# Optimization experiments

Measured on AMD Instinct MI355X. Metric: run time of the kernel, lower is better.

Reference implementation:

```python
import math
import jax, jax.numpy as jnp
import numpy as np

N_NODES = 4096
N_EDGES = 16384
N_EFEAT = 16384
L = 8          # mem_token
DIM = 512
HEAD = 8
NL = 2         # mid_num_layers
ROPE_THETA = 10000.0


def _rms(x, w, eps=1e-6):
    v = jnp.mean(jnp.square(x), axis=-1, keepdims=True)
    return x * jax.lax.rsqrt(v + eps) * w


def _rope_cos_sin(seq_len, d, theta):
    inv = 1.0 / (theta ** (jnp.arange(0, d, 2, dtype=jnp.float32) / d))
    f = jnp.outer(jnp.arange(seq_len, dtype=jnp.float32), inv)  # [L, d/2]
    emb = jnp.concatenate([f, f], axis=-1)                       # [L, d]
    return jnp.cos(emb), jnp.sin(emb)


def _rot_half(x):
    h = x.shape[-1] // 2
    return jnp.concatenate([-x[..., h:], x[..., :h]], axis=-1)


def setup_inputs() -> dict:
    key = jax.random.key(0)
    ks = jax.random.split(key, 12)
    s = 0.02
    return {
        "hidden_states": jax.random.normal(ks[0], (N_NODES + N_EFEAT, L * DIM), jnp.float32),
        "edge_index": jax.random.randint(ks[1], (2, N_EDGES), 0, N_NODES),
        "edge_map": jax.random.randint(ks[2], (N_EDGES,), 0, N_EFEAT),
        "num_node_feat": N_NODES,
        "W_qkv": jax.random.normal(ks[3], (NL, DIM, 3 * DIM), jnp.float32) * s,
        "W_e": jax.random.normal(ks[4], (NL, DIM, 2 * DIM), jnp.float32) * s,
        "W_o": jax.random.normal(ks[5], (NL, DIM, DIM), jnp.float32) * s,
        "x_norm_w": jnp.ones((NL, DIM), jnp.float32),
        "xe_norm_w": jnp.ones((NL, DIM), jnp.float32),
        "post_norm_w": jnp.ones((NL, DIM), jnp.float32),
        "ff_W1": jax.random.normal(ks[6], (NL, DIM, 2 * DIM), jnp.float32) * s,
        "ff_b1": jnp.zeros((NL, 2 * DIM), jnp.float32),
        "ff_W2": jax.random.normal(ks[7], (NL, 2 * DIM, DIM), jnp.float32) * s,
        "ff_b2": jnp.zeros((NL, DIM), jnp.float32),
    }


def reference(hidden_states, edge_index, edge_map, num_node_feat,
              W_qkv, W_e, W_o, x_norm_w, xe_norm_w, post_norm_w,
              ff_W1, ff_b1, ff_W2, ff_b2):
    n_layers, dim = W_qkv.shape[0], W_qkv.shape[1]
    n_tot = hidden_states.shape[0]
    seq = hidden_states.shape[1] // dim           # mem_token
    d = dim // HEAD                               # d_model per head
    N = int(num_node_feat)
    src, dst = edge_index[0], edge_index[1]
    cos, sin = _rope_cos_sin(seq, d, ROPE_THETA)
    cos = cos[None, :, None, :]   # [1, L, 1, d]
    sin = sin[None, :, None, :]
    inv_sqrt_d = 1.0 / math.sqrt(d)

    h = hidden_states.reshape(n_tot, seq, dim)
    for l in range(n_layers):
        x = h[:N]                        # [N, L, dim]
        xe = h[N:][edge_map]             # [E, L, dim]
        res = x
        xn = _rms(x, x_norm_w[l])
        xen = _rms(xe, xe_norm_w[l])
        q, k, v = jnp.split(jnp.einsum('nld,de->nle', xn, W_qkv[l]), 3, axis=-1)
        ek, ev = jnp.split(jnp.einsum('eld,df->elf', xen, W_e[l]), 2, axis=-1)
        # gather per-edge, fuse edge features into key/value
        qi = q[dst].reshape(-1, seq, HEAD, d)
        kj = (k[src] + ek).reshape(-1, seq, HEAD, d)
        vj = (v[src] + ev).reshape(-1, seq, HEAD, d)
        # rotary over memory-token positions
        qi = qi * cos + _rot_half(qi) * sin
        kj = kj * cos + _rot_half(kj) * sin
        alpha = jnp.einsum('elhd,elhd->elh', qi, kj) * inv_sqrt_d  # [E, L, H]
        # segment softmax over incoming edges of each destination node
        m = jax.ops.segment_max(alpha, dst, num_segments=N)
        m = jnp.where(jnp.isfinite(m), m, 0.0)
        a = jnp.exp(alpha - m[dst])
        s = jax.ops.segment_sum(a, dst, num_segments=N)
        a = a / (s[dst] + 1e-16)
        out_e = (vj * a[..., None]).reshape(-1, seq, dim)          # [E, L, dim]
        agg = jax.ops.segment_sum(out_e, dst, num_segments=N)      # [N, L, dim]
        out = res + jnp.einsum('nld,de->nle', agg, W_o[l])
        res2 = out
        o = _rms(out, post_norm_w[l])
        ff = jnp.einsum('nlf,fd->nld',
                        jax.nn.relu(jnp.einsum('nld,df->nlf', o, ff_W1[l]) + ff_b1[l]),
                        ff_W2[l]) + ff_b2[l]
        out = res2 + ff
        h = jnp.concatenate([out, h[N:]], axis=0)
    return h
```

## Files before the change

kernel.cpp:

```cpp
#include <hip/hip_runtime.h>

typedef unsigned short u16;
typedef unsigned int   u32;
typedef u16   u16x8 __attribute__((ext_vector_type(8)));
typedef __bf16 bf16x8 __attribute__((ext_vector_type(8)));
typedef float f32x4 __attribute__((ext_vector_type(4)));
typedef float f32x4v __attribute__((ext_vector_type(4)));

#define N_NODES 4096
#define N_EDGES 16384
#define N_EFEAT 16384
#define SEQ 8
#define DIM 512
#define NLAYER 2
#define NROWS_X (N_NODES*SEQ)
#define NROWS_E (N_EDGES*SEQ)

__device__ __forceinline__ float b2f(u16 u){ return __uint_as_float(((u32)u)<<16); }
__device__ __forceinline__ u16 f2b(float f){ u32 b=__float_as_uint(f); b += 0x7FFFu + ((b>>16)&1u); return (u16)(b>>16); }

__device__ __forceinline__ void gl16(const u16* g, u16* l) {
    __builtin_amdgcn_global_load_lds((const __attribute__((address_space(1))) void*)g,
                                     (__attribute__((address_space(3))) void*)l, 16, 0, 0);
}

__global__ void k_tf(const float* __restrict__ src, u16* __restrict__ dst,
                     const float* __restrict__ fold, int K, int N)
{
    int idx = blockIdx.x * 256 + threadIdx.x;
    if (idx >= K * N) return;
    int c = idx / N, j = idx - c * N;
    float v = src[idx];
    if (fold) v *= fold[c];
    dst[(size_t)j * K + c] = f2b(v);
}

__global__ void k_rowprep(const float* __restrict__ src, u16* __restrict__ dst,
                          float* __restrict__ ssout)
{
    int row  = blockIdx.x * 4 + (threadIdx.x >> 6);
    int lane = threadIdx.x & 63;
    const float* p = src + (size_t)row * DIM;
    f32x4v v0 = *(const f32x4v*)(p + lane * 8);
    f32x4v v1 = *(const f32x4v*)(p + lane * 8 + 4);
    float ss = v0[0]*v0[0]+v0[1]*v0[1]+v0[2]*v0[2]+v0[3]*v0[3]
             + v1[0]*v1[0]+v1[1]*v1[1]+v1[2]*v1[2]+v1[3]*v1[3];
    #pragma unroll
    for (int d = 1; d < 64; d <<= 1) ss += __shfl_xor(ss, d);
    if (lane == 0) ssout[row] = ss;
    u16x8 o;
    #pragma unroll
    for (int i = 0; i < 4; ++i) o[i] = f2b(v0[i]);
    #pragma unroll
    for (int i = 0; i < 4; ++i) o[4+i] = f2b(v1[i]);
    *(u16x8*)(dst + (size_t)row * DIM + lane * 8) = o;
}

__global__ void k_mark(const int* __restrict__ emap, int* __restrict__ flag)
{
    int e = blockIdx.x * 256 + threadIdx.x;
    if (e < N_EDGES) flag[emap[e]] = 1;
}
__global__ void k_scanf(const int* __restrict__ flag, int* __restrict__ newid,
                        int* __restrict__ ulist, int* __restrict__ ucnt)
{
    __shared__ int part[256];
    int t = threadIdx.x;
    int base = t * 64;
    int loc[64]; int s = 0;
    #pragma unroll
    for (int i = 0; i < 64; ++i) { loc[i] = s; s += flag[base + i]; }
    part[t] = s; __syncthreads();
    for (int d = 1; d < 256; d <<= 1) {
        int v = (t >= d) ? part[t - d] : 0;
        __syncthreads();
        part[t] += v;
        __syncthreads();
    }
    int pre = (t == 0) ? 0 : part[t - 1];
    #pragma unroll
    for (int i = 0; i < 64; ++i) {
        int m = base + i;
        int id = pre + loc[i];
        newid[m] = id;
        if (flag[m]) ulist[id] = m;
    }
    if (t == 255) ucnt[0] = part[255];
}
__global__ void k_fidx(const int* __restrict__ emap, const int* __restrict__ newid,
                       int* __restrict__ fidx)
{
    int e = blockIdx.x * 256 + threadIdx.x;
    if (e < N_EDGES) fidx[e] = newid[emap[e]];
}
__global__ void k_featprep(const float* __restrict__ hidden, const int* __restrict__ ulist,
                           const int* __restrict__ ucnt,
                           u16* __restrict__ fbf, float* __restrict__ ssout)
{
    int fr = blockIdx.x * 4 + (threadIdx.x >> 6);
    if (fr >= ucnt[0] * SEQ) return;
    int lane = threadIdx.x & 63;
    int j = fr >> 3, l = fr & 7;
    const float* p = hidden + ((size_t)(N_NODES + ulist[j]) * SEQ + l) * DIM;
    f32x4v v0 = *(const f32x4v*)(p + lane * 8);
    f32x4v v1 = *(const f32x4v*)(p + lane * 8 + 4);
    float ss = v0[0]*v0[0]+v0[1]*v0[1]+v0[2]*v0[2]+v0[3]*v0[3]
             + v1[0]*v1[0]+v1[1]*v1[1]+v1[2]*v1[2]+v1[3]*v1[3];
    #pragma unroll
    for (int d = 1; d < 64; d <<= 1) ss += __shfl_xor(ss, d);
    if (lane == 0) ssout[fr] = ss;
    u16x8 o;
    #pragma unroll
    for (int i = 0; i < 4; ++i) o[i] = f2b(v0[i]);
    #pragma unroll
    for (int i = 0; i < 4; ++i) o[4+i] = f2b(v1[i]);
    *(u16x8*)(fbf + (size_t)fr * DIM + lane * 8) = o;
}

__global__ void k_count(const int* __restrict__ dstA, int* __restrict__ cnt)
{
    int e = blockIdx.x * 256 + threadIdx.x;
    if (e < N_EDGES) atomicAdd(&cnt[dstA[e]], 1);
}
__global__ void k_scan(const int* __restrict__ cnt, int* __restrict__ off)
{
    __shared__ int part[256];
    int t = threadIdx.x;
    int base = t * 16;
    int loc[16]; int s = 0;
    #pragma unroll
    for (int i = 0; i < 16; ++i) { loc[i] = s; s += cnt[base + i]; }
    part[t] = s; __syncthreads();
    for (int d = 1; d < 256; d <<= 1) {
        int v = (t >= d) ? part[t - d] : 0;
        __syncthreads();
        part[t] += v;
        __syncthreads();
    }
    int pre = (t == 0) ? 0 : part[t - 1];
    #pragma unroll
    for (int i = 0; i < 16; ++i) off[base + i] = pre + loc[i];
    if (t == 255) off[N_NODES] = part[255];
}
__global__ void k_fill(const int* __restrict__ dstA, const int* __restrict__ off,
                       int* __restrict__ cur, int* __restrict__ elist)
{
    int e = blockIdx.x * 256 + threadIdx.x;
    if (e < N_EDGES) {
        int d = dstA[e];
        int pos = off[d] + atomicAdd(&cur[d], 1);
        elist[pos] = e;
    }
}

#define GEMM_BODY(BID, A_, B_, N_, K_, GX_, MROWS_, SSIN_, BIAS_, RELU_, RESH_, SSOUT_, OUTF_, OUTH_) \
{                                                                                   \
    int tid  = threadIdx.x;                                                         \
    int lane = tid & 63, wid = tid >> 6;                                            \
    int xcd  = (BID) & 7;                                                           \
    int ii_  = (BID) >> 3;                                                          \
    int colt = ii_ % (GX_);                                                         \
    int rowt = (ii_ / (GX_)) * 8 + xcd;                                             \
    int row0 = rowt * 128, col0 = colt * 128;                                       \
    if ((MROWS_) && row0 >= (MROWS_)[0] * SEQ) return;                              \
    int r0 = wid * 32 + (lane >> 2);                                                \
    int r1 = r0 + 16;                                                               \
    int ce0 = ((lane & 3) * 8) ^ (((r0 >> 1) & 3) << 3);                            \
    int ce1 = ((lane & 3) * 8) ^ (((r1 >> 1) & 3) << 3);                            \
    const u16* ga0 = (A_) + (size_t)(row0 + r0) * (K_) + ce0;                       \
    const u16* ga1 = (A_) + (size_t)(row0 + r1) * (K_) + ce1;                       \
    const u16* gb0 = (B_) + (size_t)(col0 + r0) * (K_) + ce0;                       \
    const u16* gb1 = (B_) + (size_t)(col0 + r1) * (K_) + ce1;                       \
    f32x4 acc[4][4];                                                                \
    _Pragma("unroll")                                                               \
    for (int m = 0; m < 4; ++m)                                                     \
        _Pragma("unroll")                                                           \
        for (int n = 0; n < 4; ++n) { f32x4 z = {0.f,0.f,0.f,0.f}; acc[m][n] = z; } \
    int wr = wid >> 1, wc = wid & 1;                                                \
    int m15 = lane & 15, g = lane >> 4;                                             \
    int arow_l = wr * 64 + m15;                                                     \
    int brow_l = wc * 64 + m15;                                                     \
    int ksw = (g * 8) ^ (((m15 >> 1) & 3) << 3);                                    \
    int NT = (K_) / 32;                                                             \
    {                                                                               \
        gl16(ga0, &ldsA[0][wid * 1024]);                                            \
        gl16(ga1, &ldsA[0][wid * 1024 + 512]);                                      \
        gl16(gb0, &ldsB[0][wid * 1024]);                                            \
        gl16(gb1, &ldsB[0][wid * 1024 + 512]);                                      \
    }                                                                               \
    int cur = 0;                                                                    \
    for (int kt = 0; kt < NT; ++kt) {                                               \
        __syncthreads();                                                            \
        if (kt + 1 < NT) {                                                          \
            int ko = (kt + 1) * 32, bf_ = cur ^ 1;                                  \
            gl16(ga0 + ko, &ldsA[bf_][wid * 1024]);                                 \
            gl16(ga1 + ko, &ldsA[bf_][wid * 1024 + 512]);                           \
            gl16(gb0 + ko, &ldsB[bf_][wid * 1024]);                                 \
            gl16(gb1 + ko, &ldsB[bf_][wid * 1024 + 512]);                           \
        }                                                                           \
        bf16x8 af[4], bfr[4];                                                       \
        _Pragma("unroll")                                                           \
        for (int m = 0; m < 4; ++m)                                                 \
            af[m] = *(const bf16x8*)&ldsA[cur][(arow_l + m * 16) * 32 + ksw];       \
        _Pragma("unroll")                                                           \
        for (int n = 0; n < 4; ++n)                                                 \
            bfr[n] = *(const bf16x8*)&ldsB[cur][(brow_l + n * 16) * 32 + ksw];      \
        _Pragma("unroll")                                                           \
        for (int m = 0; m < 4; ++m)                                                 \
            _Pragma("unroll")                                                       \
            for (int n = 0; n < 4; ++n)                                             \
                acc[m][n] = __builtin_amdgcn_mfma_f32_16x16x32_bf16(af[m], bfr[n], acc[m][n], 0, 0, 0); \
        cur ^= 1;                                                                   \
    }                                                                               \
    _Pragma("unroll")                                                               \
    for (int m = 0; m < 4; ++m) {                                                   \
        _Pragma("unroll")                                                           \
        for (int j = 0; j < 4; ++j) {                                               \
            int row = row0 + wr * 64 + m * 16 + g * 4 + j;                          \
            float sc = 0.f;                                                         \
            if (SSIN_) sc = rsqrtf((SSIN_)[row] * (1.f / (float)DIM) + 1e-6f);      \
            float ssa = 0.f;                                                        \
            _Pragma("unroll")                                                       \
            for (int n = 0; n < 4; ++n) {                                           \
                int col = col0 + wc * 64 + n * 16 + m15;                            \
                float v = acc[m][n][j];                                             \
                if (SSIN_) v *= sc;                                                 \
                if (BIAS_) v += (BIAS_)[col];                                       \
                if (RELU_) v = fmaxf(v, 0.f);                                       \
                if (RESH_) v += b2f((RESH_)[(size_t)row * (N_) + col]);             \
                if (OUTF_) (OUTF_)[(size_t)row * (N_) + col] = v;                   \
                if (OUTH_) (OUTH_)[(size_t)row * (N_) + col] = f2b(v);              \
                ssa += v * v;                                                       \
            }                                                                       \
            if (SSOUT_) {                                                           \
                ssa += __shfl_xor(ssa, 1);                                          \
                ssa += __shfl_xor(ssa, 2);                                          \
                ssa += __shfl_xor(ssa, 4);                                          \
                ssa += __shfl_xor(ssa, 8);                                          \
                if (m15 == 0) atomicAdd(&(SSOUT_)[row], ssa);                       \
            }                                                                       \
        }                                                                           \
    }                                                                               \
}

__global__ __launch_bounds__(256, 2) void k_gemm(
    const u16* __restrict__ A, const u16* __restrict__ B,
    int M, int N, int K, int gx, const int* __restrict__ mrows,
    const float* __restrict__ ssin, const float* __restrict__ bias, int relu,
    const u16* __restrict__ resH, float* __restrict__ ssout,
    float* __restrict__ outF, u16* __restrict__ outH)
{
    __shared__ u16 ldsA[2][128 * 32];
    __shared__ u16 ldsB[2][128 * 32];
    GEMM_BODY(blockIdx.x, A, B, N, K, gx, mrows, ssin, bias, relu, resH, ssout, outF, outH)
}

__global__ __launch_bounds__(256, 2) void k_gemm2(
    int nb0,
    const u16* __restrict__ A0, const u16* __restrict__ B0,
    int N0, int K0, int gx0, const int* __restrict__ mrows0,
    const float* __restrict__ ssin0, const float* __restrict__ bias0, int relu0,
    const u16* __restrict__ resH0, float* __restrict__ ssout0,
    float* __restrict__ outF0, u16* __restrict__ outH0,
    const u16* __restrict__ A1, const u16* __restrict__ B1,
    int N1, int K1, int gx1, const int* __restrict__ mrows1,
    const float* __restrict__ ssin1, const float* __restrict__ bias1, int relu1,
    const u16* __restrict__ resH1, float* __restrict__ ssout1,
    float* __restrict__ outF1, u16* __restrict__ outH1)
{
    __shared__ u16 ldsA[2][128 * 32];
    __shared__ u16 ldsB[2][128 * 32];
    if ((int)blockIdx.x < nb0) {
        GEMM_BODY(blockIdx.x, A0, B0, N0, K0, gx0, mrows0, ssin0, bias0, relu0, resH0, ssout0, outF0, outH0)
    } else {
        int bid = blockIdx.x - nb0;
        GEMM_BODY(bid, A1, B1, N1, K1, gx1, mrows1, ssin1, bias1, relu1, resH1, ssout1, outF1, outH1)
    }
}

__global__ __launch_bounds__(256, 2) void k_attn(
    const u16* __restrict__ qkv, const u16* __restrict__ ekv,
    const int* __restrict__ srcA, const int* __restrict__ fidx,
    const int* __restrict__ off, const int* __restrict__ elist,
    u16* __restrict__ agg)
{
    int n = blockIdx.x;
    int t = threadIdx.x;
    int pair = t >> 2, sub = t & 3;
    int l = pair >> 3, hd = pair & 7;
    int doff = hd * 64 + sub * 16;

    size_t qrow = ((size_t)n * SEQ + l) * 1536;
    float qi[16];
    {
        u16x8 qa = *(const u16x8*)&qkv[qrow + doff];
        u16x8 qb = *(const u16x8*)&qkv[qrow + doff + 8];
        #pragma unroll
        for (int i = 0; i < 8; ++i) { qi[i] = b2f(qa[i]); qi[i + 8] = b2f(qb[i]); }
    }

    float mrun = -INFINITY, s = 0.f;
    float av[16];
    #pragma unroll
    for (int i = 0; i < 16; ++i) av[i] = 0.f;

    int e0 = off[n], e1 = off[n + 1];
    for (int ii = e0; ii < e1; ++ii) {
        int e = elist[ii];
        int es = srcA[e];
        size_t krow = ((size_t)es * SEQ + l) * 1536 + 512;
        size_t erow = ((size_t)fidx[e] * SEQ + l) * 1024;

        u16x8 ka = *(const u16x8*)&qkv[krow + doff];
        u16x8 kb = *(const u16x8*)&qkv[krow + doff + 8];
        u16x8 ea = *(const u16x8*)&ekv[erow + doff];
        u16x8 eb = *(const u16x8*)&ekv[erow + doff + 8];

        float dot = 0.f;
        #pragma unroll
        for (int i = 0; i < 8; ++i) {
            dot += qi[i]     * (b2f(ka[i]) + b2f(ea[i]));
            dot += qi[i + 8] * (b2f(kb[i]) + b2f(eb[i]));
        }
        dot += __shfl_xor(dot, 1);
        dot += __shfl_xor(dot, 2);
        float alpha = dot * 0.125f;

        float mn = fmaxf(mrun, alpha);
        float f = expf(mrun - mn);
        float p = expf(alpha - mn);
        s = s * f + p;

        u16x8 va  = *(const u16x8*)&qkv[krow + 512 + doff];
        u16x8 vb  = *(const u16x8*)&qkv[krow + 512 + doff + 8];
        u16x8 eva = *(const u16x8*)&ekv[erow + 512 + doff];
        u16x8 evb = *(const u16x8*)&ekv[erow + 512 + doff + 8];
        #pragma unroll
        for (int i = 0; i < 8; ++i) {
            av[i]     = av[i]     * f + p * (b2f(va[i]) + b2f(eva[i]));
            av[i + 8] = av[i + 8] * f + p * (b2f(vb[i]) + b2f(evb[i]));
        }
        mrun = mn;
    }

    float inv = 1.f / (s + 1e-16f);
    size_t orow = ((size_t)n * SEQ + l) * DIM + doff;
    #pragma unroll
    for (int i = 0; i < 16; ++i) agg[orow + i] = f2b(av[i] * inv);
}

extern "C" void kernel_launch(void* const* d_in, const int* in_sizes, int n_in,
                              void* d_out, int out_size, void* d_ws, size_t ws_size,
                              hipStream_t stream)
{
    const float* hidden = (const float*)d_in[0];
    const int*   eidx   = (const int*)d_in[1];
    const int*   srcA   = eidx;
    const int*   dstA   = eidx + N_EDGES;
    const int*   emap   = (const int*)d_in[2];
    const float* W_qkv  = (const float*)d_in[4];
    const float* W_e    = (const float*)d_in[5];
    const float* W_o    = (const float*)d_in[6];
    const float* xw     = (const float*)d_in[7];
    const float* xew    = (const float*)d_in[8];
    const float* pw     = (const float*)d_in[9];
    const float* W1     = (const float*)d_in[10];
    const float* b1     = (const float*)d_in[11];
    const float* W2     = (const float*)d_in[12];
    const float* b2     = (const float*)d_in[13];

    char* w = (char*)d_ws;
    auto alloc = [&](size_t bytes) { char* p = w; w += (bytes + 255) & ~(size_t)255; return p; };
    u16*  WtQKV  = (u16*)alloc((size_t)NLAYER * 1536 * 512 * 2);
    u16*  WtE    = (u16*)alloc((size_t)NLAYER * 1024 * 512 * 2);
    u16*  WtO    = (u16*)alloc((size_t)NLAYER * 512 * 512 * 2);
    u16*  Wt1    = (u16*)alloc((size_t)NLAYER * 1024 * 512 * 2);
    u16*  Wt2    = (u16*)alloc((size_t)NLAYER * 512 * 1024 * 2);
    float* ssx0  = (float*)alloc((size_t)NROWS_X * 4);
    float* ssx1  = (float*)alloc((size_t)NROWS_X * 4);
    float* ssp0  = (float*)alloc((size_t)NROWS_X * 4);
    float* ssp1  = (float*)alloc((size_t)NROWS_X * 4);
    float* s_f   = (float*)alloc((size_t)NROWS_E * 4);
    int*  cnt    = (int*)alloc((N_NODES + 1) * 4);
    int*  off    = (int*)alloc((N_NODES + 1) * 4);
    int*  cur    = (int*)alloc(N_NODES * 4);
    int*  elist  = (int*)alloc(N_EDGES * 4);
    int*  flag   = (int*)alloc(N_EFEAT * 4);
    int*  newid  = (int*)alloc(N_EFEAT * 4);
    int*  ulist  = (int*)alloc(N_EFEAT * 4);
    int*  fidx   = (int*)alloc(N_EDGES * 4);
    int*  ucnt   = (int*)alloc(256);
    u16*  hb     = (u16*)alloc((size_t)NROWS_X * DIM * 2);
    u16*  ob     = (u16*)alloc((size_t)NROWS_X * DIM * 2);
    u16*  fbf    = (u16*)alloc((size_t)NROWS_E * DIM * 2);
    u16*  qkv    = (u16*)alloc((size_t)NROWS_X * 1536 * 2);
    u16*  aggB   = (u16*)alloc((size_t)NROWS_X * DIM * 2);
    u16*  ffmid  = (u16*)alloc((size_t)NROWS_X * 1024 * 2);
    u16*  ekv    = (u16*)((float*)d_out + (size_t)NROWS_X * DIM);
    float* ssx[2] = { ssx0, ssx1 };
    float* ssp[2] = { ssp0, ssp1 };

    for (int l = 0; l < NLAYER; ++l) {
        k_tf<<<(512*1536 + 255)/256, 256, 0, stream>>>(W_qkv + (size_t)l*512*1536, WtQKV + (size_t)l*1536*512, xw  + l*512, 512, 1536);
        k_tf<<<(512*1024 + 255)/256, 256, 0, stream>>>(W_e   + (size_t)l*512*1024, WtE   + (size_t)l*1024*512, xew + l*512, 512, 1024);
        k_tf<<<(512*512  + 255)/256, 256, 0, stream>>>(W_o   + (size_t)l*512*512,  WtO   + (size_t)l*512*512,  nullptr,    512, 512);
        k_tf<<<(512*1024 + 255)/256, 256, 0, stream>>>(W1    + (size_t)l*512*1024, Wt1   + (size_t)l*1024*512, pw  + l*512, 512, 1024);
        k_tf<<<(1024*512 + 255)/256, 256, 0, stream>>>(W2    + (size_t)l*1024*512, Wt2   + (size_t)l*512*1024, nullptr,    1024, 512);
    }
    hipMemsetAsync(ssx1, 0, NROWS_X * 4, stream);
    hipMemsetAsync(ssp0, 0, NROWS_X * 4, stream);
    hipMemsetAsync(ssp1, 0, NROWS_X * 4, stream);
    hipMemsetAsync(flag, 0, N_EFEAT * 4, stream);
    k_mark<<<N_EDGES/256, 256, 0, stream>>>(emap, flag);
    k_scanf<<<1, 256, 0, stream>>>(flag, newid, ulist, ucnt);
    k_fidx<<<N_EDGES/256, 256, 0, stream>>>(emap, newid, fidx);
    k_featprep<<<NROWS_E/4, 256, 0, stream>>>(hidden, ulist, ucnt, fbf, s_f);
    hipMemsetAsync(cnt, 0, (N_NODES + 1) * 4, stream);
    hipMemsetAsync(cur, 0, N_NODES * 4, stream);
    k_count<<<N_EDGES/256, 256, 0, stream>>>(dstA, cnt);
    k_scan<<<1, 256, 0, stream>>>(cnt, off);
    k_fill<<<N_EDGES/256, 256, 0, stream>>>(dstA, off, cur, elist);
    k_rowprep<<<NROWS_X/4, 256, 0, stream>>>(hidden, hb, ssx0);

    const int nbQ = (NROWS_X/128)*(1536/128);
    const int nbE = (NROWS_E/128)*(1024/128);

    for (int l = 0; l < NLAYER; ++l) {
        int last = (l == NLAYER - 1);
        k_gemm2<<<nbQ + nbE, 256, 0, stream>>>(nbQ,
            hb, WtQKV + (size_t)l*1536*512, 1536, 512, 1536/128, nullptr,
            ssx[l], nullptr, 0, nullptr, nullptr, nullptr, qkv,
            fbf, WtE + (size_t)l*1024*512, 1024, 512, 1024/128, ucnt,
            s_f, nullptr, 0, nullptr, nullptr, nullptr, ekv);
        k_attn<<<N_NODES, 256, 0, stream>>>(qkv, ekv, srcA, fidx, off, elist, aggB);
        k_gemm<<<(NROWS_X/128)*(512/128), 256, 0, stream>>>(aggB, WtO + (size_t)l*512*512,
            NROWS_X, 512, 512, 512/128, nullptr,
            nullptr, nullptr, 0, hb, ssp[l], nullptr, ob);
        k_gemm<<<(NROWS_X/128)*(1024/128), 256, 0, stream>>>(ob, Wt1 + (size_t)l*1024*512,
            NROWS_X, 1024, 512, 1024/128, nullptr,
            ssp[l], b1 + l*1024, 1, nullptr, nullptr, nullptr, ffmid);
        k_gemm<<<(NROWS_X/128)*(512/128), 256, 0, stream>>>(ffmid, Wt2 + (size_t)l*512*1024,
            NROWS_X, 512, 1024, 512/128, nullptr,
            nullptr, b2 + l*512, 0, ob,
            last ? nullptr : ssx[1],
            last ? (float*)d_out : nullptr,
            last ? nullptr : hb);
    }

    hipMemcpyAsync((float*)d_out + (size_t)NROWS_X * DIM, hidden + (size_t)NROWS_X * DIM,
                   (size_t)N_EDGES * SEQ * DIM * 4, hipMemcpyDeviceToDevice, stream);
}
```

Before: 1.330 ms.

## Fuse setup launches and overlap the edge-feature tail copy with the W_o GEMM

Ten per-layer weight transpose launches and four memsets become a single multi-segment kernel. The node-row and edge-feature prep kernels become one launch. The large device-to-device copy of the untouched edge-feature rows was a trailing memcpy; it now runs as extra blocks of the last layer's W_o GEMM, so the copy overlaps with compute. The copy reuses the output region that held the ekv scratch, which is safe only because attention has already consumed ekv by that point. The trade-off is that copy blocks compete with the GEMM for memory bandwidth.

```diff
diff --git a/kernel.cpp b/kernel.cpp
--- a/kernel.cpp
+++ b/kernel.cpp
@@ -24,36 +24,78 @@
                                      (__attribute__((address_space(3))) void*)l, 16, 0, 0);
 }
 
-__global__ void k_tf(const float* __restrict__ src, u16* __restrict__ dst,
-                     const float* __restrict__ fold, int K, int N)
-{
-    int idx = blockIdx.x * 256 + threadIdx.x;
-    if (idx >= K * N) return;
-    int c = idx / N, j = idx - c * N;
-    float v = src[idx];
-    if (fold) v *= fold[c];
-    dst[(size_t)j * K + c] = f2b(v);
-}
-
-__global__ void k_rowprep(const float* __restrict__ src, u16* __restrict__ dst,
-                          float* __restrict__ ssout)
-{
-    int row  = blockIdx.x * 4 + (threadIdx.x >> 6);
+#define TF_SEG(CNT, SRC, DST, FOLD, KK, NN)                                   \
+    if (b < (CNT)) {                                                          \
+        int idx = b * 256 + threadIdx.x;                                      \
+        int c = idx / (NN), j = idx - c * (NN);                               \
+        float v = (SRC)[idx];                                                 \
+        if (FOLD) v *= (FOLD)[c];                                             \
+        (DST)[(size_t)j * (KK) + c] = f2b(v);                                 \
+        return;                                                               \
+    }                                                                         \
+    b -= (CNT);
+
+__global__ void k_tfall(const float* __restrict__ Wqkv, const float* __restrict__ We,
+                        const float* __restrict__ Wo,   const float* __restrict__ W1,
+                        const float* __restrict__ W2,
+                        const float* __restrict__ xw, const float* __restrict__ xew,
+                        const float* __restrict__ pw,
+                        u16* __restrict__ WtQKV, u16* __restrict__ WtE, u16* __restrict__ WtO,
+                        u16* __restrict__ Wt1, u16* __restrict__ Wt2,
+                        float* __restrict__ z0, float* __restrict__ z1,
+                        float* __restrict__ z2, int* __restrict__ zf)
+{
+    int b = blockIdx.x;
+    if (b >= 20480) {
+        b -= 20480;
+        if (b < 128) { z0[b * 256 + threadIdx.x] = 0.f; return; }
+        b -= 128;
+        if (b < 128) { z1[b * 256 + threadIdx.x] = 0.f; return; }
+        b -= 128;
+        if (b < 128) { z2[b * 256 + threadIdx.x] = 0.f; return; }
+        b -= 128;
+        zf[b * 256 + threadIdx.x] = 0; return;
+    }
+    int l = b / 10240; b -= l * 10240;
+    TF_SEG(3072, Wqkv + (size_t)l*512*1536, WtQKV + (size_t)l*1536*512, xw  + l*512, 512, 1536)
+    TF_SEG(2048, We   + (size_t)l*512*1024, WtE   + (size_t)l*1024*512, xew + l*512, 512, 1024)
+    TF_SEG(1024, Wo   + (size_t)l*512*512,  WtO   + (size_t)l*512*512,  (const float*)nullptr, 512, 512)
+    TF_SEG(2048, W1   + (size_t)l*512*1024, Wt1   + (size_t)l*1024*512, pw  + l*512, 512, 1024)
+    TF_SEG(2048, W2   + (size_t)l*1024*512, Wt2   + (size_t)l*512*1024, (const float*)nullptr, 1024, 512)
+}
+
+__global__ void k_prep(const float* __restrict__ hidden, const int* __restrict__ ulist,
+                       const int* __restrict__ ucnt,
+                       u16* __restrict__ fbf, float* __restrict__ s_f,
+                       u16* __restrict__ hb, float* __restrict__ ssx0)
+{
     int lane = threadIdx.x & 63;
-    const float* p = src + (size_t)row * DIM;
+    const float* p;
+    u16* dst; float* ssout; int orow;
+    if (blockIdx.x < NROWS_E / 4) {
+        int fr = blockIdx.x * 4 + (threadIdx.x >> 6);
+        if (fr >= ucnt[0] * SEQ) return;
+        int j = fr >> 3, l = fr & 7;
+        p = hidden + ((size_t)(N_NODES + ulist[j]) * SEQ + l) * DIM;
+        dst = fbf + (size_t)fr * DIM; ssout = s_f; orow = fr;
+    } else {
+        int row = (blockIdx.x - NROWS_E / 4) * 4 + (threadIdx.x >> 6);
+        p = hidden + (size_t)row * DIM;
+        dst = hb + (size_t)row * DIM; ssout = ssx0; orow = row;
+    }
     f32x4v v0 = *(const f32x4v*)(p + lane * 8);
     f32x4v v1 = *(const f32x4v*)(p + lane * 8 + 4);
     float ss = v0[0]*v0[0]+v0[1]*v0[1]+v0[2]*v0[2]+v0[3]*v0[3]
              + v1[0]*v1[0]+v1[1]*v1[1]+v1[2]*v1[2]+v1[3]*v1[3];
     #pragma unroll
     for (int d = 1; d < 64; d <<= 1) ss += __shfl_xor(ss, d);
-    if (lane == 0) ssout[row] = ss;
+    if (lane == 0) ssout[orow] = ss;
     u16x8 o;
     #pragma unroll
     for (int i = 0; i < 4; ++i) o[i] = f2b(v0[i]);
     #pragma unroll
     for (int i = 0; i < 4; ++i) o[4+i] = f2b(v1[i]);
-    *(u16x8*)(dst + (size_t)row * DIM + lane * 8) = o;
+    *(u16x8*)(dst + lane * 8) = o;
 }
 
 __global__ void k_mark(const int* __restrict__ emap, int* __restrict__ flag)
@@ -92,29 +134,6 @@
 {
     int e = blockIdx.x * 256 + threadIdx.x;
     if (e < N_EDGES) fidx[e] = newid[emap[e]];
-}
-__global__ void k_featprep(const float* __restrict__ hidden, const int* __restrict__ ulist,
-                           const int* __restrict__ ucnt,
-                           u16* __restrict__ fbf, float* __restrict__ ssout)
-{
-    int fr = blockIdx.x * 4 + (threadIdx.x >> 6);
-    if (fr >= ucnt[0] * SEQ) return;
-    int lane = threadIdx.x & 63;
-    int j = fr >> 3, l = fr & 7;
-    const float* p = hidden + ((size_t)(N_NODES + ulist[j]) * SEQ + l) * DIM;
-    f32x4v v0 = *(const f32x4v*)(p + lane * 8);
-    f32x4v v1 = *(const f32x4v*)(p + lane * 8 + 4);
-    float ss = v0[0]*v0[0]+v0[1]*v0[1]+v0[2]*v0[2]+v0[3]*v0[3]
-             + v1[0]*v1[0]+v1[1]*v1[1]+v1[2]*v1[2]+v1[3]*v1[3];
-    #pragma unroll
-    for (int d = 1; d < 64; d <<= 1) ss += __shfl_xor(ss, d);
-    if (lane == 0) ssout[fr] = ss;
-    u16x8 o;
-    #pragma unroll
-    for (int i = 0; i < 4; ++i) o[i] = f2b(v0[i]);
-    #pragma unroll
-    for (int i = 0; i < 4; ++i) o[4+i] = f2b(v1[i]);
-    *(u16x8*)(fbf + (size_t)fr * DIM + lane * 8) = o;
 }
 
 __global__ void k_count(const int* __restrict__ dstA, int* __restrict__ cnt)
@@ -278,6 +297,27 @@
     }
 }
 
+__global__ __launch_bounds__(256, 2) void k_gemm_copy(
+    int nb0,
+    const u16* __restrict__ A, const u16* __restrict__ B,
+    int N, int K, int gx,
+    const float* __restrict__ ssin, const float* __restrict__ bias, int relu,
+    const u16* __restrict__ resH, float* __restrict__ ssout,
+    float* __restrict__ outF, u16* __restrict__ outH,
+    const f32x4v* __restrict__ csrc, f32x4v* __restrict__ cdst)
+{
+    __shared__ u16 ldsA[2][128 * 32];
+    __shared__ u16 ldsB[2][128 * 32];
+    if ((int)blockIdx.x < nb0) {
+        GEMM_BODY(blockIdx.x, A, B, N, K, gx, (const int*)nullptr, ssin, bias, relu, resH, ssout, outF, outH)
+    } else {
+        size_t t = (size_t)(blockIdx.x - nb0) * 256 + threadIdx.x;
+        #pragma unroll
+        for (int k = 0; k < 32; ++k)
+            cdst[t + (size_t)k * 524288] = csrc[t + (size_t)k * 524288];
+    }
+}
+
 __global__ __launch_bounds__(256, 2) void k_attn(
     const u16* __restrict__ qkv, const u16* __restrict__ ekv,
     const int* __restrict__ srcA, const int* __restrict__ fidx,
@@ -400,30 +440,21 @@
     float* ssx[2] = { ssx0, ssx1 };
     float* ssp[2] = { ssp0, ssp1 };
 
-    for (int l = 0; l < NLAYER; ++l) {
-        k_tf<<<(512*1536 + 255)/256, 256, 0, stream>>>(W_qkv + (size_t)l*512*1536, WtQKV + (size_t)l*1536*512, xw  + l*512, 512, 1536);
-        k_tf<<<(512*1024 + 255)/256, 256, 0, stream>>>(W_e   + (size_t)l*512*1024, WtE   + (size_t)l*1024*512, xew + l*512, 512, 1024);
-        k_tf<<<(512*512  + 255)/256, 256, 0, stream>>>(W_o   + (size_t)l*512*512,  WtO   + (size_t)l*512*512,  nullptr,    512, 512);
-        k_tf<<<(512*1024 + 255)/256, 256, 0, stream>>>(W1    + (size_t)l*512*1024, Wt1   + (size_t)l*1024*512, pw  + l*512, 512, 1024);
-        k_tf<<<(1024*512 + 255)/256, 256, 0, stream>>>(W2    + (size_t)l*1024*512, Wt2   + (size_t)l*512*1024, nullptr,    1024, 512);
-    }
-    hipMemsetAsync(ssx1, 0, NROWS_X * 4, stream);
-    hipMemsetAsync(ssp0, 0, NROWS_X * 4, stream);
-    hipMemsetAsync(ssp1, 0, NROWS_X * 4, stream);
-    hipMemsetAsync(flag, 0, N_EFEAT * 4, stream);
+    k_tfall<<<20928, 256, 0, stream>>>(W_qkv, W_e, W_o, W1, W2, xw, xew, pw,
+                                       WtQKV, WtE, WtO, Wt1, Wt2, ssx1, ssp0, ssp1, flag);
     k_mark<<<N_EDGES/256, 256, 0, stream>>>(emap, flag);
     k_scanf<<<1, 256, 0, stream>>>(flag, newid, ulist, ucnt);
     k_fidx<<<N_EDGES/256, 256, 0, stream>>>(emap, newid, fidx);
-    k_featprep<<<NROWS_E/4, 256, 0, stream>>>(hidden, ulist, ucnt, fbf, s_f);
+    k_prep<<<NROWS_E/4 + NROWS_X/4, 256, 0, stream>>>(hidden, ulist, ucnt, fbf, s_f, hb, ssx0);
     hipMemsetAsync(cnt, 0, (N_NODES + 1) * 4, stream);
     hipMemsetAsync(cur, 0, N_NODES * 4, stream);
     k_count<<<N_EDGES/256, 256, 0, stream>>>(dstA, cnt);
     k_scan<<<1, 256, 0, stream>>>(cnt, off);
     k_fill<<<N_EDGES/256, 256, 0, stream>>>(dstA, off, cur, elist);
-    k_rowprep<<<NROWS_X/4, 256, 0, stream>>>(hidden, hb, ssx0);
 
     const int nbQ = (NROWS_X/128)*(1536/128);
     const int nbE = (NROWS_E/128)*(1024/128);
+    const int nbW = (NROWS_X/128)*(512/128);
 
     for (int l = 0; l < NLAYER; ++l) {
         int last = (l == NLAYER - 1);
@@ -433,9 +464,17 @@
             fbf, WtE + (size_t)l*1024*512, 1024, 512, 1024/128, ucnt,
             s_f, nullptr, 0, nullptr, nullptr, nullptr, ekv);
         k_attn<<<N_NODES, 256, 0, stream>>>(qkv, ekv, srcA, fidx, off, elist, aggB);
-        k_gemm<<<(NROWS_X/128)*(512/128), 256, 0, stream>>>(aggB, WtO + (size_t)l*512*512,
-            NROWS_X, 512, 512, 512/128, nullptr,
-            nullptr, nullptr, 0, hb, ssp[l], nullptr, ob);
+        if (last) {
+            k_gemm_copy<<<nbW + 2048, 256, 0, stream>>>(nbW,
+                aggB, WtO + (size_t)l*512*512, 512, 512, 512/128,
+                nullptr, nullptr, 0, hb, ssp[l], nullptr, ob,
+                (const f32x4v*)(hidden + (size_t)NROWS_X * DIM),
+                (f32x4v*)((float*)d_out + (size_t)NROWS_X * DIM));
+        } else {
+            k_gemm<<<nbW, 256, 0, stream>>>(aggB, WtO + (size_t)l*512*512,
+                NROWS_X, 512, 512, 512/128, nullptr,
+                nullptr, nullptr, 0, hb, ssp[l], nullptr, ob);
+        }
         k_gemm<<<(NROWS_X/128)*(1024/128), 256, 0, stream>>>(ob, Wt1 + (size_t)l*1024*512,
             NROWS_X, 1024, 512, 1024/128, nullptr,
             ssp[l], b1 + l*1024, 1, nullptr, nullptr, nullptr, ffmid);
@@ -446,7 +485,4 @@
             last ? (float*)d_out : nullptr,
             last ? nullptr : hb);
     }
-
-    hipMemcpyAsync((float*)d_out + (size_t)NROWS_X * DIM, hidden + (size_t)NROWS_X * DIM,
-                   (size_t)N_EDGES * SEQ * DIM * 4, hipMemcpyDeviceToDevice, stream);
-}
+}
```

After: 1.320 ms. Within noise of the previous version (-0.8%).
